# Kernel tuning notes

Measured on AMD Instinct MI355X. Metric: run time of the kernel, lower is better.

Reference implementation:

```python
import jax, jax.numpy as jnp
import numpy as np

K = 5
K2 = K * K  # 25
SLOPE = 0.01  # torch leaky_relu default


def _unfold(x, k):
    # torch.nn.Unfold(k) on reflect-padded x: channel order c-major, then kh, kw
    b, c, h, w = x.shape
    p = k // 2
    xp = jnp.pad(x, ((0, 0), (0, 0), (p, p), (p, p)), mode='reflect')
    cols = jnp.stack([xp[:, :, i:i + h, j:j + w] for i in range(k) for j in range(k)], axis=2)
    return cols.reshape(b, c * k * k, h * w)  # (b, 3*k^2, h*w)


def _lin(x, W, b):
    # torch Linear: W is (out, in)
    return x @ W.T + b


def _lrelu(x):
    return jnp.where(x >= 0, x, SLOPE * x)


def setup_inputs() -> dict:
    key = jax.random.key(0)
    ks = iter(jax.random.split(key, 64))
    d = {}
    d['x'] = jax.random.uniform(next(ks), (4, 3, 384, 384), dtype=jnp.float32)

    def mk(name, out_f, in_f):
        d['W_' + name] = jax.random.normal(next(ks), (out_f, in_f), jnp.float32) * (1.0 / np.sqrt(in_f))
        d['b_' + name] = jax.random.normal(next(ks), (out_f,), jnp.float32) * 0.01

    mk('input', 2 * K2, 3 * K2)
    mk('h1', 3 * K2, 2 * K2)
    mk('h2', 3 * K2, 3 * K2)
    mk('h3', 2 * K2, 2 * K2)
    mk('h4', 5 * K2, 2 * K2)
    mk('h5', 2 * K2, 5 * K2)
    mk('out', 3, 2 * K2)
    # encoder(3*k^2): in -> 3*in -> in -> 3
    mk('e1', 9 * K2, 3 * K2); mk('e2', 3 * K2, 9 * K2); mk('e3', 3, 3 * K2)
    # encoder(2*k^2)
    mk('f1', 6 * K2, 2 * K2); mk('f2', 2 * K2, 6 * K2); mk('f3', 3, 2 * K2)
    # decoder(2*k^2): 3 -> out -> 3*out -> out
    mk('d1', 2 * K2, 3); mk('d2', 6 * K2, 2 * K2); mk('d3', 2 * K2, 6 * K2)
    return d


def reference(x,
              W_input, b_input, W_h1, b_h1, W_h2, b_h2, W_h3, b_h3,
              W_h4, b_h4, W_h5, b_h5, W_out, b_out,
              W_e1, b_e1, W_e2, b_e2, W_e3, b_e3,
              W_f1, b_f1, W_f2, b_f2, W_f3, b_f3,
              W_d1, b_d1, W_d2, b_d2, W_d3, b_d3):
    b, c, h, w = x.shape
    sw = jnp.transpose(_unfold(x, K), (0, 2, 1))  # (b, h*w, 3*k^2)
    x1 = _lin(sw, W_input, b_input)
    x2 = _lrelu(_lin(x1, W_h1, b_h1))
    x3 = jnp.tanh(_lin(x2, W_h2, b_h2))
    x3_enc = _lin(_lin(_lin(x3, W_e1, b_e1), W_e2, b_e2), W_e3, b_e3)
    enc2_x1 = _lin(_lin(_lin(x1, W_f1, b_f1), W_f2, b_f2), W_f3, b_f3)
    x4 = _lrelu(x3_enc + enc2_x1)
    x4_dec = _lin(_lin(_lin(_lin(x4, W_d1, b_d1), W_d2, b_d2), W_d3, b_d3), W_h3, b_h3)
    x5 = jnp.tanh(_lin(x4_dec, W_h4, b_h4))
    x6 = _lin(x5, W_h5, b_h5) - x1
    x7 = _lrelu(_lin(x6, W_out, b_out))  # (b, h*w, 3)
    return jnp.transpose(x7, (0, 2, 1)).reshape(b, c, h, w)
```

## Files before the change

kernel.cpp:

```cpp
#include <hip/hip_runtime.h>


#define IW 384
#define HW (384 * 384)
#define NPIX (4 * HW)
#define MTILE 128
#define NBLK (NPIX / MTILE)

typedef _Float16 half8 __attribute__((ext_vector_type(8)));
typedef __fp16 fp16x2 __attribute__((ext_vector_type(2)));
typedef __attribute__((ext_vector_type(4))) float f32x4;
typedef __attribute__((ext_vector_type(4))) unsigned int uint4_;

#define MFMAH(A, B, C) __builtin_amdgcn_mfma_f32_16x16x32_f16((A), (B), (C), 0, 0, 0)

#define BA   0
#define B1   64
#define B2   144
#define BEF  224
#define BD   240
#define B4   304
#define B5   432
#define BOUT 496
#define BIAS_TOT 512

#define W_A0   0
#define W_A1   2048
#define W_A2   4096
#define W_H1A  6144
#define W_H1B  8704
#define W_H2A  11264
#define W_H2B  13824
#define W_H2C  16384
#define W_EF   18944
#define W_D    24064
#define W_H4C0 28160
#define W_H5C0 30208
#define W_OUT  44544
#define W_NI   45568
#define W_TOT  47616

#define STG_BE  24320
#define STG_BF  24336

__device__ __forceinline__ float lrelu(float v) { return fmaxf(v, 0.01f * v); }

#if __has_builtin(__builtin_amdgcn_exp2f)
#define EXP2F __builtin_amdgcn_exp2f
#else
#define EXP2F __builtin_exp2f
#endif

__device__ __forceinline__ float tanh_fast(float v) {
    float e = EXP2F(v * 2.8853900817779268f);
    return __builtin_fmaf(-2.0f, __builtin_amdgcn_rcpf(e + 1.0f), 1.0f);
}

__device__ __forceinline__ unsigned short f2h_bits(float v) {
    union { _Float16 h; unsigned short s; } u; u.h = (_Float16)v; return u.s;
}
__device__ __forceinline__ float h2f_bits(unsigned short s) {
    union { _Float16 h; unsigned short s; } u; u.s = s; return (float)u.h;
}
__device__ __forceinline__ unsigned packh2(float a, float b) {
    union { fp16x2 h; unsigned u; } u;
    u.h = __builtin_amdgcn_cvt_pkrtz(a, b);
    return u.u;
}

__device__ __forceinline__ void stage(float* dst, const float* __restrict__ src,
                                      int n, int tid) {
    int n4 = n >> 2;
    float4* d = (float4*)dst;
    const float4* s = (const float4*)src;
#pragma unroll 4
    for (int i = tid; i < n4; i += 256) d[i] = s[i];
    for (int i = (n4 << 2) + tid; i < n; i += 256) dst[i] = src[i];
}

__global__ __launch_bounds__(256) void setup_all(
    const float* __restrict__ W_input, const float* __restrict__ b_input,
    const float* __restrict__ W_h1,  const float* __restrict__ b_h1,
    const float* __restrict__ W_h2,  const float* __restrict__ b_h2,
    const float* __restrict__ W_h3,  const float* __restrict__ b_h3,
    const float* __restrict__ W_h4,  const float* __restrict__ b_h4,
    const float* __restrict__ W_h5,  const float* __restrict__ b_h5,
    const float* __restrict__ W_out, const float* __restrict__ b_out,
    const float* __restrict__ W_e1,  const float* __restrict__ b_e1,
    const float* __restrict__ W_e2,  const float* __restrict__ b_e2,
    const float* __restrict__ W_e3,  const float* __restrict__ b_e3,
    const float* __restrict__ W_f1,  const float* __restrict__ b_f1,
    const float* __restrict__ W_f2,  const float* __restrict__ b_f2,
    const float* __restrict__ W_f3,  const float* __restrict__ b_f3,
    const float* __restrict__ W_d1,  const float* __restrict__ b_d1,
    const float* __restrict__ W_d2,  const float* __restrict__ b_d2,
    const float* __restrict__ W_d3,  const float* __restrict__ b_d3,
    float* __restrict__ ws)
{
    const int tid = threadIdx.x;
    const int NT = 256;
    short* wimg = (short*)(ws + BIAS_TOT);

    if (blockIdx.x < 71) {
        const int soff[17] = {W_A0,W_A1,W_A2, W_H1A,W_H1B, W_H2A,W_H2B,W_H2C,
                              W_H4C0,W_H5C0, W_H4C0+4096,W_H5C0+4096,
                              W_H4C0+8192,W_H5C0+8192, W_H4C0+12288,W_H5C0+12288,
                              W_OUT};
        const int slay[17] = {0,0,0, 1,1, 2,2,2, 6,7, 6,7, 6,7, 6,7, 8};
        const int sNT[17]  = {4,4,4, 5,5, 5,5,5, 2,4, 2,4, 2,4, 2,4, 1};
        const int sKTS[17] = {1,1,1, 1,1, 1,1,1, 2,1, 2,1, 2,1, 2,1, 2};
        const int snb[17]  = {0,0,0, 0,0, 0,0,0, 0,0, 32,0, 64,0, 96,0, 0};
        const int skb[17]  = {0,32,64, 0,32, 0,32,64, 0,0, 0,32, 0,64, 0,96, 0};

        int seg = 0, local = blockIdx.x;
        while (seg < 16 && local >= sNT[seg] * sKTS[seg]) { local -= sNT[seg] * sKTS[seg]; seg++; }
        const int kts = sKTS[seg];
        const int kt = local % kts, nt = local / kts;
        const int lay = slay[seg];
        short* dst = wimg + soff[seg] + local * 512;

#pragma unroll
        for (int t = 0; t < 2; t++) {
            int idx = tid + t * 256;
            int j = idx & 7, lane = idx >> 3;
            int slot = (lay == 0) ? ((lane >> 4) * 8 + j)
                                  : (4 * (lane >> 4) + (j & 3) + 16 * (j >> 2));
            int n = snb[seg] + nt * 16 + (lane & 15);
            int k = skb[seg] + kt * 32 + slot;
            float v = 0.0f;
            switch (lay) {
                case 0: if (n < 50  && k < 75)  v = W_input[n * 75 + k]; break;
                case 1: if (n < 75  && k < 50)  v = W_h1[n * 50 + k]; break;
                case 2: if (n < 75  && k < 75)  v = W_h2[n * 75 + k]; break;
                case 6: if (n < 125 && k < 50)  v = W_h4[n * 50 + k]; break;
                case 7: if (n < 50  && k < 125) v = W_h5[n * 125 + k]; break;
                case 8: if (n < 3   && k < 50)  v = W_out[n * 50 + k]; break;
            }
            dst[idx] = (short)f2h_bits(v);
        }
        return;
    }

    if (blockIdx.x == 74) {
        for (int i = tid; i < BIAS_TOT; i += NT) {
            if (i >= BD && i < B4) continue;
            float v = 0.0f;
            if (i < B1)        { int o = i - BA;   if (o < 50)  v = b_input[o]; }
            else if (i < B2)   { int o = i - B1;   if (o < 75)  v = b_h1[o]; }
            else if (i < BEF)  { int o = i - B2;   if (o < 75)  v = b_h2[o]; }
            else if (i < BD)   { v = 0.0f; }
            else if (i < B5)   { int o = i - B4;   if (o < 125) v = b_h4[o]; }
            else if (i < BOUT) { int o = i - B5;   if (o < 50)  v = b_h5[o]; }
            else               { int o = i - BOUT; if (o < 3)   v = b_out[o]; }
            ws[i] = v;
        }
        for (int i = tid; i < 2048; i += NT) {
            int j = i & 7, lane = (i >> 3) & 63, nt = i >> 9;
            int n = nt * 16 + (lane & 15);
            int k = (nt >> 1) * 32 + 4 * (lane >> 4) + (j & 3) + 16 * (j >> 2);
            wimg[W_NI + i] = (short)f2h_bits(k == n ? -1.0f : 0.0f);
        }
        return;
    }

    __shared__ __align__(16) float A[17500];
    __shared__ float B[675];
    __shared__ float C[256];
    __shared__ float Dd[256];
    __shared__ float Es[256];
    __shared__ float S[232];

    if (blockIdx.x == 71) {
        stage(A, W_e2, 16875, tid);
        for (int i = tid; i < 225; i += NT) { Es[i] = W_e3[i]; C[i] = b_e1[i]; }
        __syncthreads();
        for (int o = tid; o < 675; o += NT) {
            int r = o / 225, c = o % 225;
            float s0 = 0.f, s1 = 0.f, s2 = 0.f;
#pragma unroll
            for (int t = 0; t < 75; t += 3) {
                s0 += Es[r * 75 + t]     * A[t * 225 + c];
                s1 += Es[r * 75 + t + 1] * A[(t + 1) * 225 + c];
                s2 += Es[r * 75 + t + 2] * A[(t + 2) * 225 + c];
            }
            B[o] = s0 + s1 + s2;
        }
        for (int o = tid; o < 75; o += NT) {
            float s0 = 0.f, s1 = 0.f, s2 = 0.f;
#pragma unroll
            for (int t = 0; t < 225; t += 3) {
                s0 += A[o * 225 + t]     * C[t];
                s1 += A[o * 225 + t + 1] * C[t + 1];
                s2 += A[o * 225 + t + 2] * C[t + 2];
            }
            Dd[o] = b_e2[o] + s0 + s1 + s2;
        }
        __syncthreads();
        stage(A, W_e1, 16875, tid);
        __syncthreads();
        for (int o = tid; o < 225; o += NT) {
            int r = o / 75, c = o % 75;
            float s0 = 0.f, s1 = 0.f, s2 = 0.f;
#pragma unroll
            for (int t = 0; t < 225; t += 3) {
                s0 += B[r * 225 + t]     * A[t * 75 + c];
                s1 += B[r * 225 + t + 1] * A[(t + 1) * 75 + c];
                s2 += B[r * 225 + t + 2] * A[(t + 2) * 75 + c];
            }
            S[o] = s0 + s1 + s2;
        }
        for (int o = tid; o < 16; o += NT) {
            float s = 0.0f;
            if (o < 3) {
                s = b_e3[o];
                for (int t = 0; t < 75; t++) s += Es[o * 75 + t] * Dd[t];
            }
            ws[STG_BE + o] = s;
        }
        __syncthreads();
        for (int i = tid; i < 3072; i += NT) {
            int j = i & 7, lane = (i >> 3) & 63, frag = i >> 9, pl = frag & 1, kt = frag >> 1;
            int n = lane & 15;
            int k = kt * 32 + 4 * (lane >> 4) + (j & 3) + 16 * (j >> 2);
            float v = (n < 3 && k < 75) ? S[n * 75 + k] : 0.0f;
            float hi = h2f_bits(f2h_bits(v));
            wimg[W_EF + i] = (short)(pl ? f2h_bits(v - hi) : f2h_bits(v));
        }
    } else if (blockIdx.x == 72) {
        stage(A,        W_f2, 7500, tid);
        stage(A + 7500, W_f1, 7500, tid);
        for (int i = tid; i < 150; i += NT) { Es[i] = W_f3[i]; C[i] = b_f1[i]; }
        __syncthreads();
        for (int o = tid; o < 450; o += NT) {
            int r = o / 150, c = o % 150;
            float s0 = 0.f, s1 = 0.f;
#pragma unroll
            for (int t = 0; t < 50; t += 2) {
                s0 += Es[r * 50 + t]     * A[t * 150 + c];
                s1 += Es[r * 50 + t + 1] * A[(t + 1) * 150 + c];
            }
            B[o] = s0 + s1;
        }
        for (int o = tid; o < 50; o += NT) {
            float s0 = 0.f, s1 = 0.f;
#pragma unroll
            for (int t = 0; t < 150; t += 2) {
                s0 += A[o * 150 + t]     * C[t];
                s1 += A[o * 150 + t + 1] * C[t + 1];
            }
            Dd[o] = b_f2[o] + s0 + s1;
        }
        __syncthreads();
        for (int o = tid; o < 150; o += NT) {
            int r = o / 50, c = o % 50;
            float s0 = 0.f, s1 = 0.f;
#pragma unroll
            for (int t = 0; t < 150; t += 2) {
                s0 += B[r * 150 + t]     * A[7500 + t * 50 + c];
                s1 += B[r * 150 + t + 1] * A[7500 + (t + 1) * 50 + c];
            }
            S[o] = s0 + s1;
        }
        for (int o = tid; o < 16; o += NT) {
            float s = 0.0f;
            if (o < 3) {
                s = b_f3[o];
                for (int t = 0; t < 50; t++) s += Es[o * 50 + t] * Dd[t];
            }
            ws[STG_BF + o] = s;
        }
        __syncthreads();
        for (int i = tid; i < 2048; i += NT) {
            int j = i & 7, lane = (i >> 3) & 63, frag = i >> 9, pl = frag & 1, kt = frag >> 1;
            int n = lane & 15;
            int k = kt * 32 + 4 * (lane >> 4) + (j & 3) + 16 * (j >> 2);
            float v = (n < 3 && k < 50) ? S[n * 50 + k] : 0.0f;
            float hi = h2f_bits(f2h_bits(v));
            wimg[W_EF + 3072 + i] = (short)(pl ? f2h_bits(v - hi) : f2h_bits(v));
        }
    } else {
        stage(A,         W_d2, 7500, tid);
        stage(A + 7500,  W_d3, 7500, tid);
        stage(A + 15000, W_h3, 2500, tid);
        for (int i = tid; i < 150; i += NT) Es[i] = W_d1[i];
        for (int i = tid; i < 50;  i += NT) C[i] = b_d1[i];
        __syncthreads();
        for (int o = tid; o < 450; o += NT) {
            int r = o / 3, c = o % 3;
            float s0 = 0.f, s1 = 0.f;
#pragma unroll
            for (int t = 0; t < 50; t += 2) {
                s0 += A[r * 50 + t]     * Es[t * 3 + c];
                s1 += A[r * 50 + t + 1] * Es[(t + 1) * 3 + c];
            }
            B[o] = s0 + s1;
        }
        for (int o = tid; o < 150; o += NT) {
            float s0 = 0.f, s1 = 0.f;
#pragma unroll
            for (int t = 0; t < 50; t += 2) {
                s0 += A[o * 50 + t]     * C[t];
                s1 += A[o * 50 + t + 1] * C[t + 1];
            }
            Dd[o] = b_d2[o] + s0 + s1;
        }
        __syncthreads();
        for (int o = tid; o < 150; o += NT) {
            int r = o / 3, c = o % 3;
            float s0 = 0.f, s1 = 0.f;
#pragma unroll
            for (int t = 0; t < 150; t += 2) {
                s0 += A[7500 + r * 150 + t]     * B[t * 3 + c];
                s1 += A[7500 + r * 150 + t + 1] * B[(t + 1) * 3 + c];
            }
            Es[o] = s0 + s1;
        }
        for (int o = tid; o < 50; o += NT) {
            float s0 = 0.f, s1 = 0.f;
#pragma unroll
            for (int t = 0; t < 150; t += 2) {
                s0 += A[7500 + o * 150 + t]     * Dd[t];
                s1 += A[7500 + o * 150 + t + 1] * Dd[t + 1];
            }
            C[o] = b_d3[o] + s0 + s1;
        }
        __syncthreads();
        for (int o = tid; o < 150; o += NT) {
            int r = o / 3, c = o % 3;
            float s0 = 0.f, s1 = 0.f;
#pragma unroll
            for (int t = 0; t < 50; t += 2) {
                s0 += A[15000 + r * 50 + t]     * Es[t * 3 + c];
                s1 += A[15000 + r * 50 + t + 1] * Es[(t + 1) * 3 + c];
            }
            S[o] = s0 + s1;
        }
        for (int o = tid; o < 64; o += NT) {
            float v = 0.0f;
            if (o < 50) {
                float s0 = 0.f, s1 = 0.f;
#pragma unroll
                for (int t = 0; t < 50; t += 2) {
                    s0 += A[15000 + o * 50 + t]     * C[t];
                    s1 += A[15000 + o * 50 + t + 1] * C[t + 1];
                }
                v = b_h3[o] + s0 + s1;
            }
            ws[BD + o] = v;
        }
        __syncthreads();
        for (int i = tid; i < 4096; i += NT) {
            int j = i & 7, lane = (i >> 3) & 63, frag = i >> 9, pl = frag & 1, nt = frag >> 1;
            int n = nt * 16 + (lane & 15);
            int k = 4 * (lane >> 4) + (j & 3) + 16 * (j >> 2);
            float v = (n < 50 && k < 3) ? S[n * 3 + k] : 0.0f;
            float hi = h2f_bits(f2h_bits(v));
            wimg[W_D + i] = (short)(pl ? f2h_bits(v - hi) : f2h_bits(v));
        }
    }
}

__device__ __forceinline__ half8 gfragH(const short* __restrict__ wl, int off) {
    return *(const half8*)(wl + off);
}

__device__ __forceinline__ half8 packB(f32x4 lo, f32x4 hi) {
    union { unsigned u32[4]; half8 v; } u;
    u.u32[0] = packh2(lo[0], lo[1]);
    u.u32[1] = packh2(lo[2], lo[3]);
    u.u32[2] = packh2(hi[0], hi[1]);
    u.u32[3] = packh2(hi[2], hi[3]);
    return u.v;
}
__device__ __forceinline__ half8 packB1(f32x4 lo) {
    union { unsigned u32[4]; half8 v; } u;
    u.u32[0] = packh2(lo[0], lo[1]);
    u.u32[1] = packh2(lo[2], lo[3]);
    u.u32[2] = 0u; u.u32[3] = 0u;
    return u.v;
}

__device__ __forceinline__ void st16(unsigned int* p, half8 v) {
    union { half8 h; uint4_ u; } c; c.h = v;
    *(uint4_*)p = c.u;
}
__device__ __forceinline__ half8 ld16(const unsigned int* p) {
    union { half8 h; uint4_ u; } c; c.u = *(const uint4_*)p;
    return c.h;
}

__device__ __forceinline__ f32x4 lrelu4(f32x4 v) {
    v[0] = lrelu(v[0]); v[1] = lrelu(v[1]); v[2] = lrelu(v[2]); v[3] = lrelu(v[3]);
    return v;
}
__device__ __forceinline__ f32x4 tanh4(f32x4 v) {
    v[0] = tanh_fast(v[0]); v[1] = tanh_fast(v[1]);
    v[2] = tanh_fast(v[2]); v[3] = tanh_fast(v[3]);
    return v;
}

__global__ __launch_bounds__(256, 4) void fused_mfma(
    const float* __restrict__ xin,
    const float* __restrict__ ws,
    float* __restrict__ out)
{
    __shared__ float patch[1984];
    __shared__ int stab[96];
    __shared__ unsigned int x1buf[4096];

    const int tid = threadIdx.x;
    const int wv = tid >> 6;
    const int lane = tid & 63;
    const int qd = lane >> 4;
    const int mcol = lane & 15;
    const short* __restrict__ wl = (const short*)(ws + BIAS_TOT) + lane * 8;

    const int g0 = blockIdx.x * MTILE;
    const int bb = g0 / HW;
    const int p0 = g0 - bb * HW;
    const int yb = p0 / IW;
    const int xblk = p0 - yb * IW;
    const float* __restrict__ xb = xin + bb * 3 * HW;

    unsigned int* xpark = x1buf + wv * 1024 + lane * 4;

    for (int e = tid; e < 1980; e += 256) {
        int cr = e / 132;
        int i  = e - cr * 132;
        int c  = cr / 5, r = cr - c * 5;
        int ty = yb + r - 2; ty = ty < 0 ? -ty : ty; ty = (766 - ty) < ty ? 766 - ty : ty;
        int tx = xblk - 2 + i; tx = tx < 0 ? -tx : tx; tx = (766 - tx) < tx ? 766 - tx : tx;
        patch[cr * 132 + i] = xb[c * HW + ty * IW + tx];
    }
    if (tid < 96) {
        int v = 0;
        if (tid < 75) {
            int c = tid / 25, rem = tid - 25 * c;
            int rr = rem / 5, ss = rem - 5 * rr;
            v = (c * 5 + rr) * 132 + ss;
        }
        stab[tid] = v;
    }
    __syncthreads();

    half8 swf[3][2];
    {
        int st[3][8];
#pragma unroll
        for (int kt = 0; kt < 3; kt++)
#pragma unroll
            for (int j = 0; j < 8; j++)
                st[kt][j] = stab[kt * 32 + qd * 8 + j];
#pragma unroll
        for (int pt = 0; pt < 2; pt++) {
            const int xloc = wv * 32 + pt * 16 + mcol;
#pragma unroll
            for (int kt = 0; kt < 3; kt++) {
                union { unsigned u32[4]; half8 v; } u;
#pragma unroll
                for (int jj = 0; jj < 8; jj += 2) {
                    float v0 = patch[st[kt][jj]     + xloc];
                    float v1 = patch[st[kt][jj + 1] + xloc];
                    if (kt == 2) {
                        int qq0 = 64 + qd * 8 + jj;
                        v0 = (qq0     < 75) ? v0 : 0.0f;
                        v1 = (qq0 + 1 < 75) ? v1 : 0.0f;
                    }
                    u.u32[jj >> 1] = packh2(v0, v1);
                }
                swf[kt][pt] = u.v;
            }
        }
    }

    f32x4 accA[4][2];
#pragma unroll
    for (int mt = 0; mt < 4; mt++) {
        f32x4 b = *(const f32x4*)(ws + BA + mt * 16 + qd * 4);
        accA[mt][0] = b; accA[mt][1] = b;
    }
#pragma unroll
    for (int kt = 0; kt < 3; kt++)
#pragma unroll
        for (int mt = 0; mt < 4; mt++) {
            half8 w = gfragH(wl, W_A0 + kt * 2048 + mt * 512);
            accA[mt][0] = MFMAH(w, swf[kt][0], accA[mt][0]);
            accA[mt][1] = MFMAH(w, swf[kt][1], accA[mt][1]);
        }
    half8 x1f[2][2];
#pragma unroll
    for (int kt = 0; kt < 2; kt++)
#pragma unroll
        for (int pt = 0; pt < 2; pt++) {
            x1f[kt][pt] = packB(accA[2 * kt][pt], accA[2 * kt + 1][pt]);
            st16(xpark + kt * 512 + pt * 256, x1f[kt][pt]);
        }

    f32x4 acc1[5][2];
#pragma unroll
    for (int mt = 0; mt < 5; mt++) {
        f32x4 b = *(const f32x4*)(ws + B1 + mt * 16 + qd * 4);
        acc1[mt][0] = b; acc1[mt][1] = b;
    }
#pragma unroll
    for (int kt = 0; kt < 2; kt++)
#pragma unroll
        for (int mt = 0; mt < 5; mt++) {
            half8 w = gfragH(wl, W_H1A + kt * 2560 + mt * 512);
            acc1[mt][0] = MFMAH(w, x1f[kt][0], acc1[mt][0]);
            acc1[mt][1] = MFMAH(w, x1f[kt][1], acc1[mt][1]);
        }
    half8 x2f[3][2];
#pragma unroll
    for (int pt = 0; pt < 2; pt++) {
        x2f[0][pt] = packB (lrelu4(acc1[0][pt]), lrelu4(acc1[1][pt]));
        x2f[1][pt] = packB (lrelu4(acc1[2][pt]), lrelu4(acc1[3][pt]));
        x2f[2][pt] = packB1(lrelu4(acc1[4][pt]));
    }

    f32x4 acc2[5][2];
#pragma unroll
    for (int mt = 0; mt < 5; mt++) {
        f32x4 b = *(const f32x4*)(ws + B2 + mt * 16 + qd * 4);
        acc2[mt][0] = b; acc2[mt][1] = b;
    }
#pragma unroll
    for (int kt = 0; kt < 3; kt++)
#pragma unroll
        for (int mt = 0; mt < 5; mt++) {
            half8 w = gfragH(wl, W_H2A + kt * 2560 + mt * 512);
            acc2[mt][0] = MFMAH(w, x2f[kt][0], acc2[mt][0]);
            acc2[mt][1] = MFMAH(w, x2f[kt][1], acc2[mt][1]);
        }
    half8 x1r[2][2];
#pragma unroll
    for (int kt = 0; kt < 2; kt++)
#pragma unroll
        for (int pt = 0; pt < 2; pt++)
            x1r[kt][pt] = ld16(xpark + kt * 512 + pt * 256);
    half8 x3f[3][2];
#pragma unroll
    for (int pt = 0; pt < 2; pt++) {
        x3f[0][pt] = packB (tanh4(acc2[0][pt]), tanh4(acc2[1][pt]));
        x3f[1][pt] = packB (tanh4(acc2[2][pt]), tanh4(acc2[3][pt]));
        x3f[2][pt] = packB1(tanh4(acc2[4][pt]));
    }

    f32x4 accEF[2];
    {
        f32x4 be = *(const f32x4*)(ws + STG_BE + qd * 4);
        f32x4 bf = *(const f32x4*)(ws + STG_BF + qd * 4);
        f32x4 b = be + bf;
        accEF[0] = b; accEF[1] = b;
    }
#pragma unroll
    for (int kt = 0; kt < 3; kt++) {
        half8 wh = gfragH(wl, W_EF + kt * 1024);
        half8 wo = gfragH(wl, W_EF + kt * 1024 + 512);
        accEF[0] = MFMAH(wh, x3f[kt][0], accEF[0]); accEF[0] = MFMAH(wo, x3f[kt][0], accEF[0]);
        accEF[1] = MFMAH(wh, x3f[kt][1], accEF[1]); accEF[1] = MFMAH(wo, x3f[kt][1], accEF[1]);
    }
#pragma unroll
    for (int kt = 0; kt < 2; kt++) {
        half8 wh = gfragH(wl, W_EF + 3072 + kt * 1024);
        half8 wo = gfragH(wl, W_EF + 3072 + kt * 1024 + 512);
        accEF[0] = MFMAH(wh, x1r[kt][0], accEF[0]); accEF[0] = MFMAH(wo, x1r[kt][0], accEF[0]);
        accEF[1] = MFMAH(wh, x1r[kt][1], accEF[1]); accEF[1] = MFMAH(wo, x1r[kt][1], accEF[1]);
    }
    half8 x4f[2];
#pragma unroll
    for (int pt = 0; pt < 2; pt++)
        x4f[pt] = packB1(lrelu4(accEF[pt]));

    f32x4 accD[4][2];
#pragma unroll
    for (int mt = 0; mt < 4; mt++) {
        f32x4 b = *(const f32x4*)(ws + BD + mt * 16 + qd * 4);
        accD[mt][0] = b; accD[mt][1] = b;
    }
#pragma unroll
    for (int mt = 0; mt < 4; mt++) {
        half8 wh = gfragH(wl, W_D + mt * 1024);
        half8 wo = gfragH(wl, W_D + mt * 1024 + 512);
        accD[mt][0] = MFMAH(wh, x4f[0], accD[mt][0]); accD[mt][0] = MFMAH(wo, x4f[0], accD[mt][0]);
        accD[mt][1] = MFMAH(wh, x4f[1], accD[mt][1]); accD[mt][1] = MFMAH(wo, x4f[1], accD[mt][1]);
    }
    half8 xdf[2][2];
#pragma unroll
    for (int kt = 0; kt < 2; kt++)
#pragma unroll
        for (int pt = 0; pt < 2; pt++)
            xdf[kt][pt] = packB(accD[2 * kt][pt], accD[2 * kt + 1][pt]);

    f32x4 x6a[4][2];
#pragma unroll
    for (int mt = 0; mt < 4; mt++) {
        f32x4 b = *(const f32x4*)(ws + B5 + mt * 16 + qd * 4);
        half8 nI = gfragH(wl, W_NI + mt * 512);
        x6a[mt][0] = MFMAH(nI, x1r[mt >> 1][0], b);
        x6a[mt][1] = MFMAH(nI, x1r[mt >> 1][1], b);
    }

#pragma unroll
    for (int c = 0; c < 4; c++) {
        f32x4 acc5[2][2];
#pragma unroll
        for (int mt2 = 0; mt2 < 2; mt2++) {
            f32x4 b = *(const f32x4*)(ws + B4 + c * 32 + mt2 * 16 + qd * 4);
            acc5[mt2][0] = b; acc5[mt2][1] = b;
        }
#pragma unroll
        for (int kt = 0; kt < 2; kt++)
#pragma unroll
            for (int mt2 = 0; mt2 < 2; mt2++) {
                half8 w = gfragH(wl, W_H4C0 + c * 4096 + (mt2 * 2 + kt) * 512);
                acc5[mt2][0] = MFMAH(w, xdf[kt][0], acc5[mt2][0]);
                acc5[mt2][1] = MFMAH(w, xdf[kt][1], acc5[mt2][1]);
            }
        half8 chf[2];
#pragma unroll
        for (int pt = 0; pt < 2; pt++)
            chf[pt] = packB(tanh4(acc5[0][pt]), tanh4(acc5[1][pt]));
#pragma unroll
        for (int mt = 0; mt < 4; mt++) {
            half8 w = gfragH(wl, W_H5C0 + c * 4096 + mt * 512);
            x6a[mt][0] = MFMAH(w, chf[0], x6a[mt][0]);
            x6a[mt][1] = MFMAH(w, chf[1], x6a[mt][1]);
        }
    }

    f32x4 accO[2];
    {
        f32x4 b = *(const f32x4*)(ws + BOUT + qd * 4);
        accO[0] = b; accO[1] = b;
    }
#pragma unroll
    for (int kt = 0; kt < 2; kt++) {
        half8 x6f0 = packB(x6a[2 * kt][0], x6a[2 * kt + 1][0]);
        half8 x6f1 = packB(x6a[2 * kt][1], x6a[2 * kt + 1][1]);
        half8 w = gfragH(wl, W_OUT + kt * 512);
        accO[0] = MFMAH(w, x6f0, accO[0]);
        accO[1] = MFMAH(w, x6f1, accO[1]);
    }
    if (qd == 0) {
#pragma unroll
        for (int pt = 0; pt < 2; pt++) {
            int p = p0 + wv * 32 + pt * 16 + mcol;
#pragma unroll
            for (int r = 0; r < 3; r++)
                out[(bb * 3 + r) * HW + p] = lrelu(accO[pt][r]);
        }
    }
}

extern "C" void kernel_launch(void* const* d_in, const int* in_sizes, int n_in,
                              void* d_out, int out_size, void* d_ws, size_t ws_size,
                              hipStream_t stream)
{
    const float* xin = (const float*)d_in[0];
    float* ws = (float*)d_ws;

    setup_all<<<75, 256, 0, stream>>>(
        (const float*)d_in[1],  (const float*)d_in[2],
        (const float*)d_in[3],  (const float*)d_in[4],
        (const float*)d_in[5],  (const float*)d_in[6],
        (const float*)d_in[7],  (const float*)d_in[8],
        (const float*)d_in[9],  (const float*)d_in[10],
        (const float*)d_in[11], (const float*)d_in[12],
        (const float*)d_in[13], (const float*)d_in[14],
        (const float*)d_in[15], (const float*)d_in[16],
        (const float*)d_in[17], (const float*)d_in[18],
        (const float*)d_in[19], (const float*)d_in[20],
        (const float*)d_in[21], (const float*)d_in[22],
        (const float*)d_in[23], (const float*)d_in[24],
        (const float*)d_in[25], (const float*)d_in[26],
        (const float*)d_in[27], (const float*)d_in[28],
        (const float*)d_in[29], (const float*)d_in[30],
        (const float*)d_in[31], (const float*)d_in[32],
        ws);

    fused_mfma<<<NBLK, 256, 0, stream>>>(xin, ws, (float*)d_out);
}
```

Before: 235.1 us.

## Raise pixel tile to 192 per block and park decoder output in LDS

Raises the pixel tile from 128 to 192 (three 16-pixel subtiles per wave instead of two), so each weight fragment loaded from global memory feeds three MFMAs instead of two. The decoder output is now written to LDS (reusing the x1 slot once x1 has been reloaded) and read back in each h4/h5 chunk, with an asm barrier on the pointer to force the reload. This keeps register pressure in check despite the larger tile. In exchange it uses more LDS and registers per block, gives fewer blocks overall, and may lower occupancy under launch_bounds(256,4).

```diff
diff --git a/kernel.cpp b/kernel.cpp
--- a/kernel.cpp
+++ b/kernel.cpp
@@ -4,7 +4,7 @@
 #define IW 384
 #define HW (384 * 384)
 #define NPIX (4 * HW)
-#define MTILE 128
+#define MTILE 192
 #define NBLK (NPIX / MTILE)
 
 typedef _Float16 half8 __attribute__((ext_vector_type(8)));
@@ -404,9 +404,9 @@
     const float* __restrict__ ws,
     float* __restrict__ out)
 {
-    __shared__ float patch[1984];
+    __shared__ float patch[2940];
     __shared__ int stab[96];
-    __shared__ unsigned int x1buf[4096];
+    __shared__ unsigned int x1buf[6144];
 
     const int tid = threadIdx.x;
     const int wv = tid >> 6;
@@ -422,28 +422,28 @@
     const int xblk = p0 - yb * IW;
     const float* __restrict__ xb = xin + bb * 3 * HW;
 
-    unsigned int* xpark = x1buf + wv * 1024 + lane * 4;
-
-    for (int e = tid; e < 1980; e += 256) {
-        int cr = e / 132;
-        int i  = e - cr * 132;
+    unsigned int* xpark = x1buf + wv * 1536 + lane * 4;
+
+    for (int e = tid; e < 2940; e += 256) {
+        int cr = e / 196;
+        int i  = e - cr * 196;
         int c  = cr / 5, r = cr - c * 5;
         int ty = yb + r - 2; ty = ty < 0 ? -ty : ty; ty = (766 - ty) < ty ? 766 - ty : ty;
         int tx = xblk - 2 + i; tx = tx < 0 ? -tx : tx; tx = (766 - tx) < tx ? 766 - tx : tx;
-        patch[cr * 132 + i] = xb[c * HW + ty * IW + tx];
+        patch[cr * 196 + i] = xb[c * HW + ty * IW + tx];
     }
     if (tid < 96) {
         int v = 0;
         if (tid < 75) {
             int c = tid / 25, rem = tid - 25 * c;
             int rr = rem / 5, ss = rem - 5 * rr;
-            v = (c * 5 + rr) * 132 + ss;
+            v = (c * 5 + rr) * 196 + ss;
         }
         stab[tid] = v;
     }
     __syncthreads();
 
-    half8 swf[3][2];
+    half8 swf[3][3];
     {
         int st[3][8];
 #pragma unroll
@@ -452,8 +452,8 @@
             for (int j = 0; j < 8; j++)
                 st[kt][j] = stab[kt * 32 + qd * 8 + j];
 #pragma unroll
-        for (int pt = 0; pt < 2; pt++) {
-            const int xloc = wv * 32 + pt * 16 + mcol;
+        for (int pt = 0; pt < 3; pt++) {
+            const int xloc = wv * 48 + pt * 16 + mcol;
 #pragma unroll
             for (int kt = 0; kt < 3; kt++) {
                 union { unsigned u32[4]; half8 v; } u;
@@ -473,179 +473,204 @@
         }
     }
 
-    f32x4 accA[4][2];
+    f32x4 accA[4][3];
 #pragma unroll
     for (int mt = 0; mt < 4; mt++) {
         f32x4 b = *(const f32x4*)(ws + BA + mt * 16 + qd * 4);
-        accA[mt][0] = b; accA[mt][1] = b;
+        accA[mt][0] = b; accA[mt][1] = b; accA[mt][2] = b;
     }
 #pragma unroll
     for (int kt = 0; kt < 3; kt++)
 #pragma unroll
         for (int mt = 0; mt < 4; mt++) {
             half8 w = gfragH(wl, W_A0 + kt * 2048 + mt * 512);
-            accA[mt][0] = MFMAH(w, swf[kt][0], accA[mt][0]);
-            accA[mt][1] = MFMAH(w, swf[kt][1], accA[mt][1]);
-        }
-    half8 x1f[2][2];
+#pragma unroll
+            for (int pt = 0; pt < 3; pt++)
+                accA[mt][pt] = MFMAH(w, swf[kt][pt], accA[mt][pt]);
+        }
+    half8 x1f[2][3];
 #pragma unroll
     for (int kt = 0; kt < 2; kt++)
 #pragma unroll
-        for (int pt = 0; pt < 2; pt++) {
+        for (int pt = 0; pt < 3; pt++) {
             x1f[kt][pt] = packB(accA[2 * kt][pt], accA[2 * kt + 1][pt]);
-            st16(xpark + kt * 512 + pt * 256, x1f[kt][pt]);
-        }
-
-    f32x4 acc1[5][2];
+            st16(xpark + kt * 768 + pt * 256, x1f[kt][pt]);
+        }
+
+    f32x4 acc1[5][3];
 #pragma unroll
     for (int mt = 0; mt < 5; mt++) {
         f32x4 b = *(const f32x4*)(ws + B1 + mt * 16 + qd * 4);
-        acc1[mt][0] = b; acc1[mt][1] = b;
+        acc1[mt][0] = b; acc1[mt][1] = b; acc1[mt][2] = b;
     }
 #pragma unroll
     for (int kt = 0; kt < 2; kt++)
 #pragma unroll
         for (int mt = 0; mt < 5; mt++) {
             half8 w = gfragH(wl, W_H1A + kt * 2560 + mt * 512);
-            acc1[mt][0] = MFMAH(w, x1f[kt][0], acc1[mt][0]);
-            acc1[mt][1] = MFMAH(w, x1f[kt][1], acc1[mt][1]);
-        }
-    half8 x2f[3][2];
-#pragma unroll
-    for (int pt = 0; pt < 2; pt++) {
+#pragma unroll
+            for (int pt = 0; pt < 3; pt++)
+                acc1[mt][pt] = MFMAH(w, x1f[kt][pt], acc1[mt][pt]);
+        }
+    half8 x2f[3][3];
+#pragma unroll
+    for (int pt = 0; pt < 3; pt++) {
         x2f[0][pt] = packB (lrelu4(acc1[0][pt]), lrelu4(acc1[1][pt]));
         x2f[1][pt] = packB (lrelu4(acc1[2][pt]), lrelu4(acc1[3][pt]));
         x2f[2][pt] = packB1(lrelu4(acc1[4][pt]));
     }
 
-    f32x4 acc2[5][2];
+    f32x4 acc2[5][3];
 #pragma unroll
     for (int mt = 0; mt < 5; mt++) {
         f32x4 b = *(const f32x4*)(ws + B2 + mt * 16 + qd * 4);
-        acc2[mt][0] = b; acc2[mt][1] = b;
+        acc2[mt][0] = b; acc2[mt][1] = b; acc2[mt][2] = b;
     }
 #pragma unroll
     for (int kt = 0; kt < 3; kt++)
 #pragma unroll
         for (int mt = 0; mt < 5; mt++) {
             half8 w = gfragH(wl, W_H2A + kt * 2560 + mt * 512);
-            acc2[mt][0] = MFMAH(w, x2f[kt][0], acc2[mt][0]);
-            acc2[mt][1] = MFMAH(w, x2f[kt][1], acc2[mt][1]);
-        }
-    half8 x1r[2][2];
-#pragma unroll
-    for (int kt = 0; kt < 2; kt++)
-#pragma unroll
-        for (int pt = 0; pt < 2; pt++)
-            x1r[kt][pt] = ld16(xpark + kt * 512 + pt * 256);
-    half8 x3f[3][2];
-#pragma unroll
-    for (int pt = 0; pt < 2; pt++) {
+#pragma unroll
+            for (int pt = 0; pt < 3; pt++)
+                acc2[mt][pt] = MFMAH(w, x2f[kt][pt], acc2[mt][pt]);
+        }
+    half8 x3f[3][3];
+#pragma unroll
+    for (int pt = 0; pt < 3; pt++) {
         x3f[0][pt] = packB (tanh4(acc2[0][pt]), tanh4(acc2[1][pt]));
         x3f[1][pt] = packB (tanh4(acc2[2][pt]), tanh4(acc2[3][pt]));
         x3f[2][pt] = packB1(tanh4(acc2[4][pt]));
     }
-
-    f32x4 accEF[2];
+    half8 x1r[2][3];
+#pragma unroll
+    for (int kt = 0; kt < 2; kt++)
+#pragma unroll
+        for (int pt = 0; pt < 3; pt++)
+            x1r[kt][pt] = ld16(xpark + kt * 768 + pt * 256);
+
+    f32x4 accEF[3];
     {
         f32x4 be = *(const f32x4*)(ws + STG_BE + qd * 4);
         f32x4 bf = *(const f32x4*)(ws + STG_BF + qd * 4);
         f32x4 b = be + bf;
-        accEF[0] = b; accEF[1] = b;
+        accEF[0] = b; accEF[1] = b; accEF[2] = b;
     }
 #pragma unroll
     for (int kt = 0; kt < 3; kt++) {
         half8 wh = gfragH(wl, W_EF + kt * 1024);
         half8 wo = gfragH(wl, W_EF + kt * 1024 + 512);
-        accEF[0] = MFMAH(wh, x3f[kt][0], accEF[0]); accEF[0] = MFMAH(wo, x3f[kt][0], accEF[0]);
-        accEF[1] = MFMAH(wh, x3f[kt][1], accEF[1]); accEF[1] = MFMAH(wo, x3f[kt][1], accEF[1]);
+#pragma unroll
+        for (int pt = 0; pt < 3; pt++) {
+            accEF[pt] = MFMAH(wh, x3f[kt][pt], accEF[pt]);
+            accEF[pt] = MFMAH(wo, x3f[kt][pt], accEF[pt]);
+        }
     }
 #pragma unroll
     for (int kt = 0; kt < 2; kt++) {
         half8 wh = gfragH(wl, W_EF + 3072 + kt * 1024);
         half8 wo = gfragH(wl, W_EF + 3072 + kt * 1024 + 512);
-        accEF[0] = MFMAH(wh, x1r[kt][0], accEF[0]); accEF[0] = MFMAH(wo, x1r[kt][0], accEF[0]);
-        accEF[1] = MFMAH(wh, x1r[kt][1], accEF[1]); accEF[1] = MFMAH(wo, x1r[kt][1], accEF[1]);
-    }
-    half8 x4f[2];
-#pragma unroll
-    for (int pt = 0; pt < 2; pt++)
+#pragma unroll
+        for (int pt = 0; pt < 3; pt++) {
+            accEF[pt] = MFMAH(wh, x1r[kt][pt], accEF[pt]);
+            accEF[pt] = MFMAH(wo, x1r[kt][pt], accEF[pt]);
+        }
+    }
+    half8 x4f[3];
+#pragma unroll
+    for (int pt = 0; pt < 3; pt++)
         x4f[pt] = packB1(lrelu4(accEF[pt]));
 
-    f32x4 accD[4][2];
-#pragma unroll
-    for (int mt = 0; mt < 4; mt++) {
-        f32x4 b = *(const f32x4*)(ws + BD + mt * 16 + qd * 4);
-        accD[mt][0] = b; accD[mt][1] = b;
-    }
-#pragma unroll
-    for (int mt = 0; mt < 4; mt++) {
-        half8 wh = gfragH(wl, W_D + mt * 1024);
-        half8 wo = gfragH(wl, W_D + mt * 1024 + 512);
-        accD[mt][0] = MFMAH(wh, x4f[0], accD[mt][0]); accD[mt][0] = MFMAH(wo, x4f[0], accD[mt][0]);
-        accD[mt][1] = MFMAH(wh, x4f[1], accD[mt][1]); accD[mt][1] = MFMAH(wo, x4f[1], accD[mt][1]);
-    }
-    half8 xdf[2][2];
-#pragma unroll
-    for (int kt = 0; kt < 2; kt++)
-#pragma unroll
-        for (int pt = 0; pt < 2; pt++)
-            xdf[kt][pt] = packB(accD[2 * kt][pt], accD[2 * kt + 1][pt]);
-
-    f32x4 x6a[4][2];
+    f32x4 x6a[4][3];
 #pragma unroll
     for (int mt = 0; mt < 4; mt++) {
         f32x4 b = *(const f32x4*)(ws + B5 + mt * 16 + qd * 4);
         half8 nI = gfragH(wl, W_NI + mt * 512);
-        x6a[mt][0] = MFMAH(nI, x1r[mt >> 1][0], b);
-        x6a[mt][1] = MFMAH(nI, x1r[mt >> 1][1], b);
+#pragma unroll
+        for (int pt = 0; pt < 3; pt++)
+            x6a[mt][pt] = MFMAH(nI, x1r[mt >> 1][pt], b);
+    }
+
+#pragma unroll
+    for (int h = 0; h < 2; h++) {
+        f32x4 accD[2][3];
+#pragma unroll
+        for (int m2 = 0; m2 < 2; m2++) {
+            f32x4 b = *(const f32x4*)(ws + BD + (h * 2 + m2) * 16 + qd * 4);
+            accD[m2][0] = b; accD[m2][1] = b; accD[m2][2] = b;
+        }
+#pragma unroll
+        for (int m2 = 0; m2 < 2; m2++) {
+            int mt = h * 2 + m2;
+            half8 wh = gfragH(wl, W_D + mt * 1024);
+            half8 wo = gfragH(wl, W_D + mt * 1024 + 512);
+#pragma unroll
+            for (int pt = 0; pt < 3; pt++) {
+                accD[m2][pt] = MFMAH(wh, x4f[pt], accD[m2][pt]);
+                accD[m2][pt] = MFMAH(wo, x4f[pt], accD[m2][pt]);
+            }
+        }
+#pragma unroll
+        for (int pt = 0; pt < 3; pt++)
+            st16(xpark + h * 768 + pt * 256, packB(accD[0][pt], accD[1][pt]));
     }
 
 #pragma unroll
     for (int c = 0; c < 4; c++) {
-        f32x4 acc5[2][2];
+        const unsigned int* xr = xpark;
+        asm volatile("" : "+v"(xr));
+        half8 xd[2][3];
+#pragma unroll
+        for (int kt = 0; kt < 2; kt++)
+#pragma unroll
+            for (int pt = 0; pt < 3; pt++)
+                xd[kt][pt] = ld16(xr + kt * 768 + pt * 256);
+        f32x4 acc5[2][3];
 #pragma unroll
         for (int mt2 = 0; mt2 < 2; mt2++) {
             f32x4 b = *(const f32x4*)(ws + B4 + c * 32 + mt2 * 16 + qd * 4);
-            acc5[mt2][0] = b; acc5[mt2][1] = b;
+            acc5[mt2][0] = b; acc5[mt2][1] = b; acc5[mt2][2] = b;
         }
 #pragma unroll
         for (int kt = 0; kt < 2; kt++)
 #pragma unroll
             for (int mt2 = 0; mt2 < 2; mt2++) {
                 half8 w = gfragH(wl, W_H4C0 + c * 4096 + (mt2 * 2 + kt) * 512);
-                acc5[mt2][0] = MFMAH(w, xdf[kt][0], acc5[mt2][0]);
-                acc5[mt2][1] = MFMAH(w, xdf[kt][1], acc5[mt2][1]);
-            }
-        half8 chf[2];
-#pragma unroll
-        for (int pt = 0; pt < 2; pt++)
+#pragma unroll
+                for (int pt = 0; pt < 3; pt++)
+                    acc5[mt2][pt] = MFMAH(w, xd[kt][pt], acc5[mt2][pt]);
+            }
+        half8 chf[3];
+#pragma unroll
+        for (int pt = 0; pt < 3; pt++)
             chf[pt] = packB(tanh4(acc5[0][pt]), tanh4(acc5[1][pt]));
 #pragma unroll
         for (int mt = 0; mt < 4; mt++) {
             half8 w = gfragH(wl, W_H5C0 + c * 4096 + mt * 512);
-            x6a[mt][0] = MFMAH(w, chf[0], x6a[mt][0]);
-            x6a[mt][1] = MFMAH(w, chf[1], x6a[mt][1]);
-        }
-    }
-
-    f32x4 accO[2];
+#pragma unroll
+            for (int pt = 0; pt < 3; pt++)
+                x6a[mt][pt] = MFMAH(w, chf[pt], x6a[mt][pt]);
+        }
+    }
+
+    f32x4 accO[3];
     {
         f32x4 b = *(const f32x4*)(ws + BOUT + qd * 4);
-        accO[0] = b; accO[1] = b;
+        accO[0] = b; accO[1] = b; accO[2] = b;
     }
 #pragma unroll
     for (int kt = 0; kt < 2; kt++) {
-        half8 x6f0 = packB(x6a[2 * kt][0], x6a[2 * kt + 1][0]);
-        half8 x6f1 = packB(x6a[2 * kt][1], x6a[2 * kt + 1][1]);
         half8 w = gfragH(wl, W_OUT + kt * 512);
-        accO[0] = MFMAH(w, x6f0, accO[0]);
-        accO[1] = MFMAH(w, x6f1, accO[1]);
+#pragma unroll
+        for (int pt = 0; pt < 3; pt++) {
+            half8 x6f = packB(x6a[2 * kt][pt], x6a[2 * kt + 1][pt]);
+            accO[pt] = MFMAH(w, x6f, accO[pt]);
+        }
     }
     if (qd == 0) {
 #pragma unroll
-        for (int pt = 0; pt < 2; pt++) {
-            int p = p0 + wv * 32 + pt * 16 + mcol;
+        for (int pt = 0; pt < 3; pt++) {
+            int p = p0 + wv * 48 + pt * 16 + mcol;
 #pragma unroll
             for (int r = 0; r < 3; r++)
                 out[(bb * 3 + r) * HW + p] = lrelu(accO[pt][r]);
```

Measured after the change: 241.4 us. 1.03x slower.
